# Kernel optimization log

Measured on AMD Instinct MI355X. Metric: run time of the kernel, lower is better.

Reference implementation:

```python
import jax, jax.numpy as jnp
import numpy as np

B, CIN, T, H, W = 1, 256, 64, 32, 32
A, G = 8, 8
SCALES = jnp.array([1., 2., 4., 8., 16., 32., 64., 128.], dtype=jnp.float32)
FEAT_STRIDE = 8.0
NMS_TOP_N = 100
NMS_THRESH = 0.7
MIN_SIZE = 4.0
POS_THR, NEG_THR = 0.7, 0.3
NEG_INF = -1e9


def _conv3d(x, w, b, strides):
    y = jax.lax.conv_general_dilated(
        x, w, window_strides=strides, padding=[(1, 1)] * 3,
        dimension_numbers=('NCDHW', 'OIDHW', 'NCDHW'))
    return y + b[None, :, None, None, None]


def _iou(a, b):
    # 1D interval IoU; a, b broadcastable [..., 2] = (start, end)
    inter = jnp.maximum(jnp.minimum(a[..., 1], b[..., 1]) - jnp.maximum(a[..., 0], b[..., 0]), 0.0)
    union = (a[..., 1] - a[..., 0]) + (b[..., 1] - b[..., 0]) - inter
    return inter / jnp.maximum(union, 1e-6)


def _nms(boxes, scores):
    # greedy 1D NMS: boxes [N,2], scores [N] -> top NMS_TOP_N (zero-padded)
    n = scores.shape[0]
    def step(sc, _):
        i = jnp.argmax(sc)
        s, box = sc[i], boxes[i]
        sup = (_iou(box[None], boxes) > NMS_THRESH) | (jnp.arange(n) == i)
        return jnp.where(sup, NEG_INF, sc), (box, s)
    _, (kb, ks) = jax.lax.scan(step, scores, None, length=NMS_TOP_N)
    keep = ks > NEG_INF * 0.5
    return jnp.where(keep[:, None], kb, 0.0), jnp.where(keep, ks, 0.0)


def _forward(base_feat, gt_chunks, video_len, c1w, c1b, c2w, c2b, sw, sb, dw, db):
    bsz = base_feat.shape[0]
    x = _conv3d(base_feat, c1w, c1b, (1, 2, 2))
    x = _conv3d(x, c2w, c2b, (1, 2, 2))
    feat = jnp.max(x, axis=(3, 4))                       # AdaptiveMaxPool3d((None,1,1)) -> [B,512,T]
    tlen = feat.shape[2]
    score_logit = (jnp.einsum('oc,bct->bot', sw, feat) + sb[None, :, None]).reshape(bsz, 2, A, tlen)
    delta = (jnp.einsum('oc,bct->bot', dw, feat) + db[None, :, None]).reshape(bsz, 2, A, tlen)
    prob = jax.nn.softmax(score_logit, axis=1)
    logp = jax.nn.log_softmax(score_logit, axis=1)

    # anchors: A lengths x T temporal positions, flattened as a*T + t
    anchor_len = FEAT_STRIDE * SCALES                                    # [A]
    centers = (jnp.arange(tlen, dtype=jnp.float32) + 0.5) * FEAT_STRIDE  # [T]
    a_start = centers[None, :] - anchor_len[:, None] / 2                 # [A,T]
    a_end = centers[None, :] + anchor_len[:, None] / 2
    anchors = jnp.stack([a_start, a_end], -1).reshape(-1, 2)             # [N,2]
    N = A * tlen

    # ---- proposal decode + NMS ----
    dc, dl = delta[:, 0], delta[:, 1]                                    # [B,A,T]
    pc = centers[None, None, :] + dc * anchor_len[None, :, None]
    pl = anchor_len[None, :, None] * jnp.exp(jnp.clip(dl, -10.0, 10.0))
    lim = tlen * FEAT_STRIDE
    ps = jnp.clip(pc - pl / 2, 0.0, lim)
    pe = jnp.clip(pc + pl / 2, 0.0, lim)
    boxes = jnp.stack([ps, pe], -1).reshape(bsz, N, 2)
    fg = prob[:, 1].reshape(bsz, N)
    fg = jnp.where((pe - ps).reshape(bsz, N) >= MIN_SIZE, fg, NEG_INF)
    prop_coord, prop_score = jax.vmap(_nms)(boxes, fg)

    # ---- IoU-based label assignment ----
    ious = _iou(anchors[None, :, None, :], gt_chunks[:, None, :, :])     # [B,N,G]
    max_iou = ious.max(-1)
    arg = ious.argmax(-1)                                                # [B,N]
    label = jnp.where(max_iou < NEG_THR, 0, -1)
    label = jnp.where(max_iou >= POS_THR, 1, label)
    best = ious.argmax(1)                                                # best anchor per gt [B,G]
    bidx = jnp.arange(bsz)[:, None]
    label = label.at[bidx, best].set(1)
    vl = video_len.astype(jnp.float32)[:, None]
    inside = (anchors[None, :, 0] >= 0.0) & (anchors[None, :, 1] <= vl)
    label = jnp.where(inside, label, -1)

    matched = gt_chunks[bidx, arg]                                       # [B,N,2]
    gc = (matched[..., 0] + matched[..., 1]) / 2
    gl = jnp.maximum(matched[..., 1] - matched[..., 0], 1e-6)
    ac = (anchors[:, 0] + anchors[:, 1]) / 2
    al = anchors[:, 1] - anchors[:, 0]
    reg_label = jnp.stack([(gc - ac[None]) / al[None], jnp.log(gl / al[None])], -1)
    reg_label = jax.lax.stop_gradient(reg_label)                          # targets carry no grad

    # ---- losses ----
    logp2 = logp.reshape(bsz, 2, N).transpose(0, 2, 1)                   # [B,N,2]
    lab = jnp.maximum(label, 0)
    nll = -jnp.take_along_axis(logp2, lab[..., None], axis=2)[..., 0]
    mask = (label >= 0).astype(jnp.float32)
    cls_loss = (nll * mask).sum() / jnp.maximum(mask.sum(), 1.0)

    delta2 = delta.reshape(bsz, 2, N).transpose(0, 2, 1)                 # [B,N,2]
    d = delta2 - reg_label
    sl1 = jnp.where(jnp.abs(d) < 1.0, 0.5 * d * d, jnp.abs(d) - 0.5).sum(-1)
    pos = (label == 1).astype(jnp.float32)
    reg_loss = (sl1 * pos).sum() / jnp.maximum(pos.sum(), 1.0)
    return prop_coord, prop_score, cls_loss, reg_loss


def setup_inputs() -> dict:
    key = jax.random.key(0)
    ks = jax.random.split(key, 8)
    base_feat = jax.random.normal(ks[0], (B, CIN, T, H, W), jnp.float32)
    starts = jax.random.uniform(ks[1], (B, G), minval=0.0, maxval=448.0)
    lens = jax.random.uniform(ks[2], (B, G), minval=8.0, maxval=64.0)
    gt_chunks = jnp.stack([starts, jnp.clip(starts + lens, 0.0, T * FEAT_STRIDE)], -1)
    video_len = jnp.full((B,), int(T * FEAT_STRIDE), jnp.int32)
    s = 0.02
    return dict(
        base_feat=base_feat, gt_chunks=gt_chunks, video_len=video_len,
        conv1_w=jax.random.normal(ks[3], (512, CIN, 3, 3, 3), jnp.float32) * s,
        conv1_b=jnp.zeros((512,), jnp.float32),
        conv2_w=jax.random.normal(ks[4], (512, 512, 3, 3, 3), jnp.float32) * s,
        conv2_b=jnp.zeros((512,), jnp.float32),
        score_w=jax.random.normal(ks[5], (2 * A, 512), jnp.float32) * s,
        score_b=jnp.zeros((2 * A,), jnp.float32),
        delta_w=jax.random.normal(ks[6], (2 * A, 512), jnp.float32) * s,
        delta_b=jnp.zeros((2 * A,), jnp.float32),
    )


def reference(base_feat, gt_chunks, video_len, conv1_w, conv1_b, conv2_w, conv2_b, score_w, score_b, delta_w, delta_b):
    return _forward(base_feat, gt_chunks, video_len, conv1_w, conv1_b, conv2_w, conv2_b, score_w, score_b, delta_w, delta_b)
```

## Files before the change

kernel.cpp:

```cpp
#include <hip/hip_runtime.h>

typedef __attribute__((ext_vector_type(8))) _Float16 half8;
typedef __attribute__((ext_vector_type(4))) _Float16 half4;
typedef __attribute__((ext_vector_type(4))) float floatx4;

#define DI __device__ __forceinline__

DI void gl_lds16(const void* g, void* l) {
    __builtin_amdgcn_global_load_lds(
        (__attribute__((address_space(1))) void*)(g),
        (__attribute__((address_space(3))) void*)(l), 16, 0, 0);
}


__global__ __launch_bounds__(256) void wt_split_t(
        const float* __restrict__ w1, _Float16* __restrict__ w1I,
        const float* __restrict__ w2, _Float16* __restrict__ w2I,
        float* __restrict__ zp) {
    __shared__ float L[13824];
    const int b = blockIdx.x;
    const int tid = threadIdx.x;
    if (b == 0 && tid < 64) zp[tid] = 0.0f;
    if (b < 512) {
        const float* src = w1 + (size_t)b * 6912;
        for (int idx = tid; idx < 6912; idx += 256) L[idx] = src[idx] * 64.0f;
        __syncthreads();
        for (int c = tid; c < 864; c += 256) {
            const int tap = c >> 5, o = c & 31;
            half8 h, l;
#pragma unroll
            for (int j = 0; j < 8; ++j) {
                const float x = L[(o * 8 + j) * 27 + tap];
                const _Float16 hh = (_Float16)x;
                h[j] = hh; l[j] = (_Float16)(x - (float)hh);
            }
            const size_t off = (size_t)b * 13824 + (size_t)(tap * 8 + (o >> 2)) * 64 + (o & 3) * 8;
            *(half8*)&w1I[off] = h;
            *(half8*)&w1I[off + 32] = l;
        }
    } else {
        const float* src = w2 + (size_t)(b - 512) * 13824;
        for (int idx = tid; idx < 13824; idx += 256) L[idx] = src[idx] * 64.0f;
        __syncthreads();
        for (int c = tid; c < 1728; c += 256) {
            const int tap = c >> 6, o = c & 63;
            half8 h, l;
#pragma unroll
            for (int j = 0; j < 8; ++j) {
                const float x = L[(o * 8 + j) * 27 + tap];
                const _Float16 hh = (_Float16)x;
                h[j] = hh; l[j] = (_Float16)(x - (float)hh);
            }
            const size_t off = (size_t)(b - 512) * 27648 + (size_t)(tap * 16 + (o >> 2)) * 64 + (o & 3) * 8;
            *(half8*)&w2I[off] = h;
            *(half8*)&w2I[off + 32] = l;
        }
    }
}

__global__ __launch_bounds__(256) void in_split(const float* __restrict__ in,
                                                _Float16* __restrict__ oI) {
    __shared__ float T[128 * 65];
    const int hb = blockIdx.x;
    const int s0 = blockIdx.y * 64;
    const int tid = threadIdx.x;
    const int cil = tid >> 1, part = tid & 1;
    const float* src = in + (size_t)(hb * 128 + cil) * 65536 + s0 + part * 32;
    float v[32];
#pragma unroll
    for (int q = 0; q < 8; ++q) *(float4*)(v + q * 4) = *(const float4*)(src + q * 4);
#pragma unroll
    for (int j = 0; j < 32; ++j) T[cil * 65 + part * 32 + j] = v[j];
    __syncthreads();
#pragma unroll
    for (int k = 0; k < 4; ++k) {
        const int c = tid + k * 256;
        const int sp = c >> 4, ol = c & 15;
        half8 h, l;
#pragma unroll
        for (int j = 0; j < 8; ++j) {
            const float x = T[(ol * 8 + j) * 65 + sp];
            const _Float16 hh = (_Float16)x;
            h[j] = hh; l[j] = (_Float16)(x - (float)hh);
        }
        const int og = hb * 16 + ol;
        const size_t off = (size_t)(s0 + sp) * 512 + (size_t)(og >> 2) * 64 + (og & 3) * 8;
        *(half8*)&oI[off] = h;
        *(half8*)&oI[off + 32] = l;
    }
}

__global__ __launch_bounds__(256, 2) void conv1_mfma(
        const _Float16* __restrict__ xI, const _Float16* __restrict__ wI,
        const float* __restrict__ b1, const _Float16* __restrict__ zp,
        _Float16* __restrict__ yI) {
    __shared__ __align__(16) _Float16 A2[2][128 * 64];
    __shared__ __align__(16) _Float16 B2[2][128 * 64];
    const int tid = threadIdx.x;
    const int co_blk = blockIdx.x;
    const int t = blockIdx.y;
    const int h0 = blockIdx.z * 8;
    const int wid = tid >> 6, lane = tid & 63;
    const int wm = wid & 1, wn = wid >> 1;
    const int ml = lane & 15, ql = lane >> 4;
    const int cs0 = (ql ^ (ml & 7)) * 8;
    const int cs1 = ((4 + ql) ^ (ml & 7)) * 8;
    const int sl = lane & 7, rl = lane >> 3;
    const int lc = sl ^ rl;
    size_t aoff[4]; int dstq[4], ih2[4], iw2[4];
    const size_t wbo = (size_t)co_blk * 128 * 13824;
#pragma unroll
    for (int q = 0; q < 4; ++q) {
        const int row = (q * 4 + wid) * 8 + rl;
        aoff[q] = wbo + (size_t)row * 13824 + lc * 8;
        dstq[q] = (q * 4 + wid) * 512 + lane * 8;
        const int h = h0 + (row >> 4), w = row & 15;
        ih2[q] = 2 * h - 1; iw2[q] = 2 * w - 1;
    }

    floatx4 zz = {0.f, 0.f, 0.f, 0.f};
    floatx4 acc[4][4];
#pragma unroll
    for (int i = 0; i < 4; ++i)
#pragma unroll
        for (int j = 0; j < 4; ++j) acc[i][j] = zz;

    auto stage = [&](int kt, int kh, int kw, int cb, int bi) {
        const int tap = (kt * 3 + kh) * 3 + kw;
        const size_t ab = (size_t)(tap * 8 + cb) * 64;
        _Float16* Ad = A2[bi]; _Float16* Bd = B2[bi];
        const int it = t + kt - 1;
        const bool tok = ((unsigned)it < 64u);
#pragma unroll
        for (int q = 0; q < 4; ++q) {
            gl_lds16(wI + aoff[q] + ab, &Ad[dstq[q]]);
            const int ih = ih2[q] + kh, iw = iw2[q] + kw;
            const bool ok = tok && ((unsigned)ih < 32u) && ((unsigned)iw < 32u);
            const _Float16* src = ok
                ? (xI + (size_t)(it * 1024 + ih * 32 + iw) * 512 + cb * 64 + lc * 8)
                : (zp + lc * 8);
            gl_lds16(src, &Bd[dstq[q]]);
        }
    };

    int kt = 0, kh = 0, kw = 0, cb = 0;
    stage(0, 0, 0, 0, 0);
    kw = 1;
    for (int i = 0; i < 216; ++i) {
        __syncthreads();
        if (i + 1 < 216) {
            stage(kt, kh, kw, cb, (i + 1) & 1);
            if (++kw == 3) { kw = 0; if (++kh == 3) { kh = 0; if (++kt == 3) { kt = 0; ++cb; } } }
        }
        const _Float16* Ab = A2[i & 1];
        const _Float16* Bb = B2[i & 1];
        half8 ah[4], alo[4], bh8[4], blo[4];
#pragma unroll
        for (int mi = 0; mi < 4; ++mi) {
            ah[mi]  = *(const half8*)&Ab[(wm * 64 + mi * 16 + ml) * 64 + cs0];
            alo[mi] = *(const half8*)&Ab[(wm * 64 + mi * 16 + ml) * 64 + cs1];
        }
#pragma unroll
        for (int ni = 0; ni < 4; ++ni) {
            bh8[ni] = *(const half8*)&Bb[(wn * 64 + ni * 16 + ml) * 64 + cs0];
            blo[ni] = *(const half8*)&Bb[(wn * 64 + ni * 16 + ml) * 64 + cs1];
        }
#pragma unroll
        for (int mi = 0; mi < 4; ++mi)
#pragma unroll
            for (int ni = 0; ni < 4; ++ni) {
                acc[mi][ni] = __builtin_amdgcn_mfma_f32_16x16x32_f16(ah[mi],  bh8[ni], acc[mi][ni], 0, 0, 0);
                acc[mi][ni] = __builtin_amdgcn_mfma_f32_16x16x32_f16(ah[mi],  blo[ni], acc[mi][ni], 0, 0, 0);
                acc[mi][ni] = __builtin_amdgcn_mfma_f32_16x16x32_f16(alo[mi], bh8[ni], acc[mi][ni], 0, 0, 0);
            }
    }

    const int qr = ql * 4;
#pragma unroll
    for (int mi = 0; mi < 4; ++mi) {
        const int co = co_blk * 128 + wm * 64 + mi * 16 + qr;
#pragma unroll
        for (int ni = 0; ni < 4; ++ni) {
            const int n = wn * 64 + ni * 16 + ml;
            const int h = h0 + (n >> 4), w = n & 15;
            const size_t base = ((size_t)t * 256 + h * 16 + w) * 1024
                              + (size_t)(co >> 5) * 64 + (co & 31);
            half4 hv, lv;
#pragma unroll
            for (int r = 0; r < 4; ++r) {
                const float v = acc[mi][ni][r] * 0.015625f + b1[co + r];
                const _Float16 hb = (_Float16)v;
                hv[r] = hb;
                lv[r] = (_Float16)(v - (float)hb);
            }
            *(half4*)(yI + base) = hv;
            *(half4*)(yI + base + 32) = lv;
        }
    }
}

__global__ __launch_bounds__(256, 2) void conv2_mfma(
        const _Float16* __restrict__ xI, const _Float16* __restrict__ wI,
        const _Float16* __restrict__ zp,
        float* __restrict__ x2p) {
    __shared__ __align__(16) _Float16 A2[2][128 * 64];
    __shared__ __align__(16) _Float16 B2[2][128 * 64];
    const int tid = threadIdx.x;
    const int co_blk = blockIdx.x;
    const int tp = blockIdx.y;
    const int ks = blockIdx.z;
    const int wid = tid >> 6, lane = tid & 63;
    const int wm = wid & 1, wn = wid >> 1;
    const int ml = lane & 15, ql = lane >> 4;
    const int cs0 = (ql ^ (ml & 7)) * 8;
    const int cs1 = ((4 + ql) ^ (ml & 7)) * 8;
    const int sl = lane & 7, rl = lane >> 3;
    const int lc = sl ^ rl;
    size_t aoff[4]; int dstq[4], ih2[4], iw2[4], tl4[4];
    const size_t wbo = (size_t)co_blk * 128 * 27648;
#pragma unroll
    for (int q = 0; q < 4; ++q) {
        const int row = (q * 4 + wid) * 8 + rl;
        aoff[q] = wbo + (size_t)row * 27648 + lc * 8;
        dstq[q] = (q * 4 + wid) * 512 + lane * 8;
        const int sp = row & 63;
        tl4[q] = row >> 6;
        ih2[q] = 2 * (sp >> 3) - 1; iw2[q] = 2 * (sp & 7) - 1;
    }

    floatx4 zz = {0.f, 0.f, 0.f, 0.f};
    floatx4 acc[4][4];
#pragma unroll
    for (int i = 0; i < 4; ++i)
#pragma unroll
        for (int j = 0; j < 4; ++j) acc[i][j] = zz;

    auto stage = [&](int kt, int kh, int kw, int cb, int bi) {
        const int tap = (kt * 3 + kh) * 3 + kw;
        const size_t ab = (size_t)(tap * 16 + cb) * 64;
        _Float16* Ad = A2[bi]; _Float16* Bd = B2[bi];
#pragma unroll
        for (int q = 0; q < 4; ++q) {
            gl_lds16(wI + aoff[q] + ab, &Ad[dstq[q]]);
            const int it = tp * 2 + tl4[q] + kt - 1;
            const int ih = ih2[q] + kh, iw = iw2[q] + kw;
            const bool ok = ((unsigned)it < 64u) && ((unsigned)ih < 16u) && ((unsigned)iw < 16u);
            const _Float16* src = ok
                ? (xI + (size_t)(it * 256 + ih * 16 + iw) * 1024 + cb * 64 + lc * 8)
                : (zp + lc * 8);
            gl_lds16(src, &Bd[dstq[q]]);
        }
    };

    int kt = 0, kh = 0, kw = 0, cb = ks * 4;
    stage(0, 0, 0, cb, 0);
    kw = 1;
    for (int i = 0; i < 108; ++i) {
        __syncthreads();
        if (i + 1 < 108) {
            stage(kt, kh, kw, cb, (i + 1) & 1);
            if (++kw == 3) { kw = 0; if (++kh == 3) { kh = 0; if (++kt == 3) { kt = 0; ++cb; } } }
        }
        const _Float16* Ab = A2[i & 1];
        const _Float16* Bb = B2[i & 1];
        half8 ah[4], alo[4], bh8[4], blo[4];
#pragma unroll
        for (int mi = 0; mi < 4; ++mi) {
            ah[mi]  = *(const half8*)&Ab[(wm * 64 + mi * 16 + ml) * 64 + cs0];
            alo[mi] = *(const half8*)&Ab[(wm * 64 + mi * 16 + ml) * 64 + cs1];
        }
#pragma unroll
        for (int ni = 0; ni < 4; ++ni) {
            bh8[ni] = *(const half8*)&Bb[(wn * 64 + ni * 16 + ml) * 64 + cs0];
            blo[ni] = *(const half8*)&Bb[(wn * 64 + ni * 16 + ml) * 64 + cs1];
        }
#pragma unroll
        for (int mi = 0; mi < 4; ++mi)
#pragma unroll
            for (int ni = 0; ni < 4; ++ni) {
                acc[mi][ni] = __builtin_amdgcn_mfma_f32_16x16x32_f16(ah[mi],  bh8[ni], acc[mi][ni], 0, 0, 0);
                acc[mi][ni] = __builtin_amdgcn_mfma_f32_16x16x32_f16(ah[mi],  blo[ni], acc[mi][ni], 0, 0, 0);
                acc[mi][ni] = __builtin_amdgcn_mfma_f32_16x16x32_f16(alo[mi], bh8[ni], acc[mi][ni], 0, 0, 0);
            }
    }

    const int qr = ql * 4;
#pragma unroll
    for (int mi = 0; mi < 4; ++mi) {
        const int co = co_blk * 128 + wm * 64 + mi * 16 + qr;
#pragma unroll
        for (int ni = 0; ni < 4; ++ni) {
            const int n = wn * 64 + ni * 16 + ml;
            const int ng = tp * 128 + n;
            float4 v;
            v.x = acc[mi][ni][0]; v.y = acc[mi][ni][1];
            v.z = acc[mi][ni][2]; v.w = acc[mi][ni][3];
            *(float4*)&x2p[((size_t)ks * 4096 + ng) * 512 + co] = v;
        }
    }
}

__global__ __launch_bounds__(256) void feat_head(
        const float* __restrict__ x2p, const float* __restrict__ b2,
        const float* __restrict__ sw, const float* __restrict__ sb,
        const float* __restrict__ dw, const float* __restrict__ db,
        float* __restrict__ scoreL, float* __restrict__ deltaL) {
    __shared__ float fr[512];
    __shared__ float partial[32][8];
    const int t = blockIdx.x, tid = threadIdx.x;
#pragma unroll
    for (int cc = 0; cc < 2; ++cc) {
        const int c = tid + cc * 256;
        float mx = -3.4e38f;
        for (int sp = 0; sp < 64; ++sp) {
            const size_t ng = (size_t)t * 64 + sp;
            const float s = x2p[ng * 512 + c]
                          + x2p[((size_t)4096 + ng) * 512 + c]
                          + x2p[((size_t)8192 + ng) * 512 + c]
                          + x2p[((size_t)12288 + ng) * 512 + c];
            mx = fmaxf(mx, s);
        }
        fr[c] = mx * 0.015625f + b2[c];
    }
    __syncthreads();
    const int o = tid & 31, part = tid >> 5;
    const float* wrow = (o < 16) ? (sw + (size_t)o * 512) : (dw + (size_t)(o - 16) * 512);
    float s = 0.f;
    const int j0 = part * 64;
#pragma unroll 16
    for (int j = 0; j < 64; ++j) s += wrow[j0 + j] * fr[j0 + j];
    partial[o][part] = s;
    __syncthreads();
    if (tid < 32) {
        float tot = 0.f;
#pragma unroll
        for (int p = 0; p < 8; ++p) tot += partial[tid][p];
        tot += (tid < 16) ? sb[tid] : db[tid - 16];
        if (tid < 16) scoreL[tid * 64 + t] = tot;
        else deltaL[(tid - 16) * 64 + t] = tot;
    }
}

__global__ void nms_loss_kernel(const float* __restrict__ scoreL,
                                const float* __restrict__ deltaL,
                                const float* __restrict__ gt,
                                const int* __restrict__ video_len,
                                float* __restrict__ out) {
    const int lane = threadIdx.x & 63;
    float gsv[8], gev[8];
#pragma unroll
    for (int g = 0; g < 8; ++g) { gsv[g] = gt[2 * g]; gev[g] = gt[2 * g + 1]; }
    const float center = ((float)lane + 0.5f) * 8.0f;
    float psv[8], pev[8], fg[8], l0v[8], l1v[8], dcv[8], dlv[8];
#pragma unroll
    for (int j = 0; j < 8; ++j) {
        const float s0 = scoreL[j * 64 + lane], s1 = scoreL[(8 + j) * 64 + lane];
        const float mm = fmaxf(s0, s1);
        const float lse = mm + logf(expf(s0 - mm) + expf(s1 - mm));
        l0v[j] = s0 - lse; l1v[j] = s1 - lse;
        const float dc = deltaL[j * 64 + lane], dl = deltaL[(8 + j) * 64 + lane];
        dcv[j] = dc; dlv[j] = dl;
        const float alen = 8.0f * (float)(1 << j);
        const float pc = center + dc * alen;
        const float pl = alen * expf(fminf(fmaxf(dl, -10.0f), 10.0f));
        const float ps = fminf(fmaxf(pc - pl * 0.5f, 0.0f), 512.0f);
        const float pe = fminf(fmaxf(pc + pl * 0.5f, 0.0f), 512.0f);
        psv[j] = ps; pev[j] = pe;
        fg[j] = ((pe - ps) >= 4.0f) ? expf(l1v[j]) : -1e9f;
    }
    for (int itn = 0; itn < 100; ++itn) {
        float v = fg[0]; int idx = lane;
#pragma unroll
        for (int j = 1; j < 8; ++j) if (fg[j] > v) { v = fg[j]; idx = lane + 64 * j; }
#pragma unroll
        for (int off = 32; off > 0; off >>= 1) {
            const float ov = __shfl_down(v, off);
            const int oi = __shfl_down(idx, off);
            if (ov > v || (ov == v && oi < idx)) { v = ov; idx = oi; }
        }
        v = __shfl(v, 0); idx = __shfl(idx, 0);
        const int wj = idx >> 6, wl = idx & 63;
        float bw0 = 0.f, bw1 = 0.f;
#pragma unroll
        for (int j = 0; j < 8; ++j) if (j == wj) { bw0 = psv[j]; bw1 = pev[j]; }
        const float b0 = __shfl(bw0, wl);
        const float b1 = __shfl(bw1, wl);
        if (lane == 0) {
            const bool kept = v > -5e8f;
            out[2 * itn] = kept ? b0 : 0.0f;
            out[2 * itn + 1] = kept ? b1 : 0.0f;
            out[200 + itn] = kept ? v : 0.0f;
        }
#pragma unroll
        for (int j = 0; j < 8; ++j) {
            const int n = lane + 64 * j;
            const float inter = fmaxf(fminf(b1, pev[j]) - fmaxf(b0, psv[j]), 0.0f);
            const float uni = (b1 - b0) + (pev[j] - psv[j]) - inter;
            const float iou = inter / fmaxf(uni, 1e-6f);
            if (iou > 0.7f || n == idx) fg[j] = -1e9f;
        }
    }
    int labv[8], aggv[8];
#pragma unroll
    for (int j = 0; j < 8; ++j) {
        const float alen = 8.0f * (float)(1 << j);
        const float as_ = center - alen * 0.5f, ae_ = center + alen * 0.5f;
        float mx = -1.0f; int ag = 0;
#pragma unroll
        for (int g = 0; g < 8; ++g) {
            const float inter = fmaxf(fminf(ae_, gev[g]) - fmaxf(as_, gsv[g]), 0.0f);
            const float uni = (ae_ - as_) + (gev[g] - gsv[g]) - inter;
            const float iou = inter / fmaxf(uni, 1e-6f);
            if (iou > mx) { mx = iou; ag = g; }
        }
        labv[j] = (mx < 0.3f) ? 0 : ((mx >= 0.7f) ? 1 : -1);
        aggv[j] = ag;
    }
    for (int g = 0; g < 8; ++g) {
        float v = -1.0f; int idx = 0;
#pragma unroll
        for (int j = 0; j < 8; ++j) {
            const int n = lane + 64 * j;
            const float alen = 8.0f * (float)(1 << j);
            const float as_ = center - alen * 0.5f, ae_ = center + alen * 0.5f;
            const float inter = fmaxf(fminf(ae_, gev[g]) - fmaxf(as_, gsv[g]), 0.0f);
            const float uni = (ae_ - as_) + (gev[g] - gsv[g]) - inter;
            const float iou = inter / fmaxf(uni, 1e-6f);
            if (iou > v || (iou == v && n < idx)) { v = iou; idx = n; }
        }
#pragma unroll
        for (int off = 32; off > 0; off >>= 1) {
            const float ov = __shfl_down(v, off);
            const int oi = __shfl_down(idx, off);
            if (ov > v || (ov == v && oi < idx)) { v = ov; idx = oi; }
        }
        idx = __shfl(idx, 0);
#pragma unroll
        for (int j = 0; j < 8; ++j)
            if (lane == (idx & 63) && j == (idx >> 6)) labv[j] = 1;
    }
    const float vl = (float)video_len[0];
    float nll_s = 0.f, msk_s = 0.f, reg_s = 0.f, pos_s = 0.f;
#pragma unroll
    for (int j = 0; j < 8; ++j) {
        const float alen = 8.0f * (float)(1 << j);
        const float as_ = center - alen * 0.5f, ae_ = center + alen * 0.5f;
        int l = labv[j];
        if (!((as_ >= 0.0f) && (ae_ <= vl))) l = -1;
        if (l >= 0) {
            msk_s += 1.0f;
            nll_s -= (l == 1) ? l1v[j] : l0v[j];
            if (l == 1) {
                pos_s += 1.0f;
                float gcv = 0.f, glv = 0.f;
#pragma unroll
                for (int g = 0; g < 8; ++g)
                    if (g == aggv[j]) {
                        gcv = (gsv[g] + gev[g]) * 0.5f;
                        glv = fmaxf(gev[g] - gsv[g], 1e-6f);
                    }
                const float r0 = (gcv - center) / alen;
                const float r1 = logf(glv / alen);
                const float d0 = dcv[j] - r0, d1 = dlv[j] - r1;
                float s = (fabsf(d0) < 1.0f) ? (0.5f * d0 * d0) : (fabsf(d0) - 0.5f);
                s += (fabsf(d1) < 1.0f) ? (0.5f * d1 * d1) : (fabsf(d1) - 0.5f);
                reg_s += s;
            }
        }
    }
    float sums[4] = {nll_s, msk_s, reg_s, pos_s};
#pragma unroll
    for (int k = 0; k < 4; ++k)
#pragma unroll
        for (int off = 32; off > 0; off >>= 1) sums[k] += __shfl_down(sums[k], off);
    if (lane == 0) {
        out[300] = sums[0] / fmaxf(sums[1], 1.0f);
        out[301] = sums[2] / fmaxf(sums[3], 1.0f);
    }
}

extern "C" void kernel_launch(void* const* d_in, const int* in_sizes, int n_in,
                              void* d_out, int out_size, void* d_ws, size_t ws_size,
                              hipStream_t stream) {
    const float* base_feat = (const float*)d_in[0];
    const float* gt        = (const float*)d_in[1];
    const int*   video_len = (const int*)d_in[2];
    const float* w1        = (const float*)d_in[3];
    const float* b1        = (const float*)d_in[4];
    const float* w2        = (const float*)d_in[5];
    const float* b2        = (const float*)d_in[6];
    const float* sw        = (const float*)d_in[7];
    const float* sb        = (const float*)d_in[8];
    const float* dw        = (const float*)d_in[9];
    const float* db        = (const float*)d_in[10];

    char* ws = (char*)d_ws;
    _Float16* w1I = (_Float16*)ws;  ws += (size_t)512 * 13824 * 2;
    _Float16* w2I = (_Float16*)ws;  ws += (size_t)512 * 27648 * 2;
    _Float16* inI = (_Float16*)ws;  ws += (size_t)65536 * 512 * 2;
    _Float16* x1I = (_Float16*)ws;  ws += (size_t)16384 * 1024 * 2;
    float* scoreL = (float*)ws;     ws += (size_t)16 * 64 * 4;
    float* deltaL = (float*)ws;     ws += (size_t)16 * 64 * 4;
    float* zpage  = (float*)ws;     ws += (size_t)64 * 4;
    float* x2p = (float*)inI;

    wt_split_t<<<1024, 256, 0, stream>>>(w1, w1I, w2, w2I, zpage);
    in_split<<<dim3(2, 1024), 256, 0, stream>>>(base_feat, inI);
    conv1_mfma<<<dim3(4, 64, 2), 256, 0, stream>>>(inI, w1I, b1,
                                                   (const _Float16*)zpage, x1I);
    conv2_mfma<<<dim3(4, 32, 4), 256, 0, stream>>>(x1I, w2I,
                                                   (const _Float16*)zpage, x2p);
    feat_head<<<64, 256, 0, stream>>>(x2p, b2, sw, sb, dw, db, scoreL, deltaL);
    nms_loss_kernel<<<1, 64, 0, stream>>>(scoreL, deltaL, gt, video_len,
                                          (float*)d_out);
}
```

Before: 772.0 us.

## Switch conv kernels to 32x32x16 MFMA tiles with hoisted address math

```diff
diff --git a/kernel.cpp b/kernel.cpp
--- a/kernel.cpp
+++ b/kernel.cpp
@@ -2,7 +2,7 @@
 
 typedef __attribute__((ext_vector_type(8))) _Float16 half8;
 typedef __attribute__((ext_vector_type(4))) _Float16 half4;
-typedef __attribute__((ext_vector_type(4))) float floatx4;
+typedef __attribute__((ext_vector_type(16))) float floatx16;
 
 #define DI __device__ __forceinline__
 
@@ -102,100 +102,126 @@
     const int h0 = blockIdx.z * 8;
     const int wid = tid >> 6, lane = tid & 63;
     const int wm = wid & 1, wn = wid >> 1;
-    const int ml = lane & 15, ql = lane >> 4;
-    const int cs0 = (ql ^ (ml & 7)) * 8;
-    const int cs1 = ((4 + ql) ^ (ml & 7)) * 8;
+    const int r5 = lane & 31, h5 = lane >> 5, l7 = lane & 7;
     const int sl = lane & 7, rl = lane >> 3;
     const int lc = sl ^ rl;
-    size_t aoff[4]; int dstq[4], ih2[4], iw2[4];
+
+    const _Float16* wA[4]; const _Float16* bB[4];
+    int dstq[4]; bool hok[4], wok[4];
     const size_t wbo = (size_t)co_blk * 128 * 13824;
 #pragma unroll
     for (int q = 0; q < 4; ++q) {
         const int row = (q * 4 + wid) * 8 + rl;
-        aoff[q] = wbo + (size_t)row * 13824 + lc * 8;
+        wA[q] = wI + wbo + (size_t)row * 13824 + lc * 8;
         dstq[q] = (q * 4 + wid) * 512 + lane * 8;
         const int h = h0 + (row >> 4), w = row & 15;
-        ih2[q] = 2 * h - 1; iw2[q] = 2 * w - 1;
-    }
-
-    floatx4 zz = {0.f, 0.f, 0.f, 0.f};
-    floatx4 acc[4][4];
-#pragma unroll
-    for (int i = 0; i < 4; ++i)
-#pragma unroll
-        for (int j = 0; j < 4; ++j) acc[i][j] = zz;
-
-    auto stage = [&](int kt, int kh, int kw, int cb, int bi) {
-        const int tap = (kt * 3 + kh) * 3 + kw;
-        const size_t ab = (size_t)(tap * 8 + cb) * 64;
-        _Float16* Ad = A2[bi]; _Float16* Bd = B2[bi];
+        const int ih2 = 2 * h - 1, iw2 = 2 * w - 1;
+        hok[q] = (ih2 >= 0); wok[q] = (iw2 >= 0);
+        bB[q] = xI + (ptrdiff_t)(ih2 * 32 + iw2) * 512 + lc * 8;
+    }
+    const _Float16* zpl = zp + lc * 8;
+    const int cs0 = (h5 ^ l7) * 8;
+
+    floatx16 acc[2][2];
+#pragma unroll
+    for (int mi = 0; mi < 2; ++mi)
+#pragma unroll
+        for (int ni = 0; ni < 2; ++ni)
+#pragma unroll
+            for (int e = 0; e < 16; ++e) acc[mi][ni][e] = 0.0f;
+
+    auto stage = [&](int kt, int cb, int KH, int KW, _Float16* Ad, _Float16* Bd) {
         const int it = t + kt - 1;
         const bool tok = ((unsigned)it < 64u);
+        const size_t ab = (size_t)(((kt * 9 + KH * 3 + KW) * 8 + cb) * 64);
+        const ptrdiff_t boff = (ptrdiff_t)it * 524288 + KH * 16384 + KW * 512 + cb * 64;
 #pragma unroll
         for (int q = 0; q < 4; ++q) {
-            gl_lds16(wI + aoff[q] + ab, &Ad[dstq[q]]);
-            const int ih = ih2[q] + kh, iw = iw2[q] + kw;
-            const bool ok = tok && ((unsigned)ih < 32u) && ((unsigned)iw < 32u);
-            const _Float16* src = ok
-                ? (xI + (size_t)(it * 1024 + ih * 32 + iw) * 512 + cb * 64 + lc * 8)
-                : (zp + lc * 8);
-            gl_lds16(src, &Bd[dstq[q]]);
+            gl_lds16(wA[q] + ab, &Ad[dstq[q]]);
+            const bool ok = tok && (KH > 0 || hok[q]) && (KW > 0 || wok[q]);
+            const _Float16* s = ok ? (bB[q] + boff) : zpl;
+            gl_lds16(s, &Bd[dstq[q]]);
         }
     };
 
-    int kt = 0, kh = 0, kw = 0, cb = 0;
-    stage(0, 0, 0, 0, 0);
-    kw = 1;
-    for (int i = 0; i < 216; ++i) {
-        __syncthreads();
-        if (i + 1 < 216) {
-            stage(kt, kh, kw, cb, (i + 1) & 1);
-            if (++kw == 3) { kw = 0; if (++kh == 3) { kh = 0; if (++kt == 3) { kt = 0; ++cb; } } }
-        }
-        const _Float16* Ab = A2[i & 1];
-        const _Float16* Bb = B2[i & 1];
-        half8 ah[4], alo[4], bh8[4], blo[4];
-#pragma unroll
-        for (int mi = 0; mi < 4; ++mi) {
-            ah[mi]  = *(const half8*)&Ab[(wm * 64 + mi * 16 + ml) * 64 + cs0];
-            alo[mi] = *(const half8*)&Ab[(wm * 64 + mi * 16 + ml) * 64 + cs1];
-        }
-#pragma unroll
-        for (int ni = 0; ni < 4; ++ni) {
-            bh8[ni] = *(const half8*)&Bb[(wn * 64 + ni * 16 + ml) * 64 + cs0];
-            blo[ni] = *(const half8*)&Bb[(wn * 64 + ni * 16 + ml) * 64 + cs1];
-        }
-#pragma unroll
-        for (int mi = 0; mi < 4; ++mi)
-#pragma unroll
-            for (int ni = 0; ni < 4; ++ni) {
-                acc[mi][ni] = __builtin_amdgcn_mfma_f32_16x16x32_f16(ah[mi],  bh8[ni], acc[mi][ni], 0, 0, 0);
-                acc[mi][ni] = __builtin_amdgcn_mfma_f32_16x16x32_f16(ah[mi],  blo[ni], acc[mi][ni], 0, 0, 0);
-                acc[mi][ni] = __builtin_amdgcn_mfma_f32_16x16x32_f16(alo[mi], bh8[ni], acc[mi][ni], 0, 0, 0);
-            }
-    }
-
-    const int qr = ql * 4;
-#pragma unroll
-    for (int mi = 0; mi < 4; ++mi) {
-        const int co = co_blk * 128 + wm * 64 + mi * 16 + qr;
-#pragma unroll
-        for (int ni = 0; ni < 4; ++ni) {
-            const int n = wn * 64 + ni * 16 + ml;
-            const int h = h0 + (n >> 4), w = n & 15;
-            const size_t base = ((size_t)t * 256 + h * 16 + w) * 1024
-                              + (size_t)(co >> 5) * 64 + (co & 31);
-            half4 hv, lv;
-#pragma unroll
-            for (int r = 0; r < 4; ++r) {
-                const float v = acc[mi][ni][r] * 0.015625f + b1[co + r];
-                const _Float16 hb = (_Float16)v;
-                hv[r] = hb;
-                lv[r] = (_Float16)(v - (float)hb);
-            }
-            *(half4*)(yI + base) = hv;
-            *(half4*)(yI + base + 32) = lv;
-        }
+    stage(0, 0, 0, 0, A2[0], B2[0]);
+    for (int o = 0; o < 24; ++o) {
+        const int cb = o / 3, kt = o - cb * 3;
+#pragma unroll
+        for (int j = 0; j < 9; ++j) {
+            __syncthreads();
+            const int par = (o + j) & 1;
+            if (j < 8) {
+                stage(kt, cb, (j + 1) / 3, (j + 1) % 3, A2[par ^ 1], B2[par ^ 1]);
+            } else if (o < 23) {
+                stage((o + 1) % 3, (o + 1) / 3, 0, 0, A2[par ^ 1], B2[par ^ 1]);
+            }
+            const _Float16* Ab = A2[par];
+            const _Float16* Bb = B2[par];
+            half8 a_h[2][2], a_l[2][2], b_h[2][2], b_l[2][2];
+#pragma unroll
+            for (int mi = 0; mi < 2; ++mi) {
+                const _Float16* pa = &Ab[(wm * 64 + mi * 32 + r5) * 64];
+                const _Float16* pb = &Bb[(wn * 64 + mi * 32 + r5) * 64];
+#pragma unroll
+                for (int k = 0; k < 2; ++k) {
+                    const int cs = cs0 ^ (k * 16);
+                    a_h[mi][k] = *(const half8*)&pa[cs];
+                    a_l[mi][k] = *(const half8*)&pa[cs ^ 32];
+                    b_h[mi][k] = *(const half8*)&pb[cs];
+                    b_l[mi][k] = *(const half8*)&pb[cs ^ 32];
+                }
+            }
+            __builtin_amdgcn_s_setprio(1);
+#pragma unroll
+            for (int k = 0; k < 2; ++k) {
+#pragma unroll
+                for (int mi = 0; mi < 2; ++mi)
+#pragma unroll
+                    for (int ni = 0; ni < 2; ++ni)
+                        acc[mi][ni] = __builtin_amdgcn_mfma_f32_32x32x16_f16(
+                            a_h[mi][k], b_h[ni][k], acc[mi][ni], 0, 0, 0);
+#pragma unroll
+                for (int mi = 0; mi < 2; ++mi)
+#pragma unroll
+                    for (int ni = 0; ni < 2; ++ni)
+                        acc[mi][ni] = __builtin_amdgcn_mfma_f32_32x32x16_f16(
+                            a_h[mi][k], b_l[ni][k], acc[mi][ni], 0, 0, 0);
+#pragma unroll
+                for (int mi = 0; mi < 2; ++mi)
+#pragma unroll
+                    for (int ni = 0; ni < 2; ++ni)
+                        acc[mi][ni] = __builtin_amdgcn_mfma_f32_32x32x16_f16(
+                            a_l[mi][k], b_h[ni][k], acc[mi][ni], 0, 0, 0);
+            }
+            __builtin_amdgcn_s_setprio(0);
+        }
+    }
+
+#pragma unroll
+    for (int ni = 0; ni < 2; ++ni) {
+        const int n = wn * 64 + ni * 32 + r5;
+        const int h = h0 + (n >> 4), w = n & 15;
+        const size_t spb = ((size_t)t * 256 + h * 16 + w) * 1024;
+#pragma unroll
+        for (int mi = 0; mi < 2; ++mi)
+#pragma unroll
+            for (int g = 0; g < 4; ++g) {
+                const int co = co_blk * 128 + wm * 64 + mi * 32 + g * 8 + h5 * 4;
+                const float4 bv = *(const float4*)&b1[co];
+                half4 hv, lv;
+#pragma unroll
+                for (int r = 0; r < 4; ++r) {
+                    const float bb = (r == 0) ? bv.x : (r == 1) ? bv.y : (r == 2) ? bv.z : bv.w;
+                    const float v = acc[mi][ni][g * 4 + r] * 0.015625f + bb;
+                    const _Float16 hb = (_Float16)v;
+                    hv[r] = hb;
+                    lv[r] = (_Float16)(v - (float)hb);
+                }
+                const size_t base = spb + (size_t)(co >> 5) * 64 + (co & 31);
+                *(half4*)(yI + base) = hv;
+                *(half4*)(yI + base + 32) = lv;
+            }
     }
 }
 
@@ -211,92 +237,116 @@
     const int ks = blockIdx.z;
     const int wid = tid >> 6, lane = tid & 63;
     const int wm = wid & 1, wn = wid >> 1;
-    const int ml = lane & 15, ql = lane >> 4;
-    const int cs0 = (ql ^ (ml & 7)) * 8;
-    const int cs1 = ((4 + ql) ^ (ml & 7)) * 8;
+    const int r5 = lane & 31, h5 = lane >> 5, l7 = lane & 7;
     const int sl = lane & 7, rl = lane >> 3;
     const int lc = sl ^ rl;
-    size_t aoff[4]; int dstq[4], ih2[4], iw2[4], tl4[4];
+
+    const _Float16* wA[4]; const _Float16* bB[4];
+    int dstq[4], itv[4]; bool hok[4], wok[4];
     const size_t wbo = (size_t)co_blk * 128 * 27648;
 #pragma unroll
     for (int q = 0; q < 4; ++q) {
         const int row = (q * 4 + wid) * 8 + rl;
-        aoff[q] = wbo + (size_t)row * 27648 + lc * 8;
+        wA[q] = wI + wbo + (size_t)row * 27648 + lc * 8;
         dstq[q] = (q * 4 + wid) * 512 + lane * 8;
         const int sp = row & 63;
-        tl4[q] = row >> 6;
-        ih2[q] = 2 * (sp >> 3) - 1; iw2[q] = 2 * (sp & 7) - 1;
-    }
-
-    floatx4 zz = {0.f, 0.f, 0.f, 0.f};
-    floatx4 acc[4][4];
-#pragma unroll
-    for (int i = 0; i < 4; ++i)
-#pragma unroll
-        for (int j = 0; j < 4; ++j) acc[i][j] = zz;
-
-    auto stage = [&](int kt, int kh, int kw, int cb, int bi) {
-        const int tap = (kt * 3 + kh) * 3 + kw;
-        const size_t ab = (size_t)(tap * 16 + cb) * 64;
-        _Float16* Ad = A2[bi]; _Float16* Bd = B2[bi];
+        itv[q] = tp * 2 + (row >> 6) - 1;
+        const int ih2 = 2 * (sp >> 3) - 1, iw2 = 2 * (sp & 7) - 1;
+        hok[q] = (ih2 >= 0); wok[q] = (iw2 >= 0);
+        bB[q] = xI + (ptrdiff_t)((itv[q] * 256 + ih2 * 16 + iw2) * 1024) + lc * 8;
+    }
+    const _Float16* zpl = zp + lc * 8;
+    const int cs0 = (h5 ^ l7) * 8;
+
+    floatx16 acc[2][2];
+#pragma unroll
+    for (int mi = 0; mi < 2; ++mi)
+#pragma unroll
+        for (int ni = 0; ni < 2; ++ni)
+#pragma unroll
+            for (int e = 0; e < 16; ++e) acc[mi][ni][e] = 0.0f;
+
+    auto stage = [&](int kt, int cb, int KH, int KW, _Float16* Ad, _Float16* Bd) {
+        const size_t ab = (size_t)(((kt * 9 + KH * 3 + KW) * 16 + cb) * 64);
+        const ptrdiff_t boff = (ptrdiff_t)kt * 262144 + KH * 16384 + KW * 1024 + cb * 64;
 #pragma unroll
         for (int q = 0; q < 4; ++q) {
-            gl_lds16(wI + aoff[q] + ab, &Ad[dstq[q]]);
-            const int it = tp * 2 + tl4[q] + kt - 1;
-            const int ih = ih2[q] + kh, iw = iw2[q] + kw;
-            const bool ok = ((unsigned)it < 64u) && ((unsigned)ih < 16u) && ((unsigned)iw < 16u);
-            const _Float16* src = ok
-                ? (xI + (size_t)(it * 256 + ih * 16 + iw) * 1024 + cb * 64 + lc * 8)
-                : (zp + lc * 8);
-            gl_lds16(src, &Bd[dstq[q]]);
+            gl_lds16(wA[q] + ab, &Ad[dstq[q]]);
+            const bool ok = ((unsigned)(itv[q] + kt) < 64u)
+                         && (KH > 0 || hok[q]) && (KW > 0 || wok[q]);
+            const _Float16* s = ok ? (bB[q] + boff) : zpl;
+            gl_lds16(s, &Bd[dstq[q]]);
         }
     };
 
-    int kt = 0, kh = 0, kw = 0, cb = ks * 4;
-    stage(0, 0, 0, cb, 0);
-    kw = 1;
-    for (int i = 0; i < 108; ++i) {
-        __syncthreads();
-        if (i + 1 < 108) {
-            stage(kt, kh, kw, cb, (i + 1) & 1);
-            if (++kw == 3) { kw = 0; if (++kh == 3) { kh = 0; if (++kt == 3) { kt = 0; ++cb; } } }
-        }
-        const _Float16* Ab = A2[i & 1];
-        const _Float16* Bb = B2[i & 1];
-        half8 ah[4], alo[4], bh8[4], blo[4];
-#pragma unroll
-        for (int mi = 0; mi < 4; ++mi) {
-            ah[mi]  = *(const half8*)&Ab[(wm * 64 + mi * 16 + ml) * 64 + cs0];
-            alo[mi] = *(const half8*)&Ab[(wm * 64 + mi * 16 + ml) * 64 + cs1];
-        }
-#pragma unroll
-        for (int ni = 0; ni < 4; ++ni) {
-            bh8[ni] = *(const half8*)&Bb[(wn * 64 + ni * 16 + ml) * 64 + cs0];
-            blo[ni] = *(const half8*)&Bb[(wn * 64 + ni * 16 + ml) * 64 + cs1];
-        }
-#pragma unroll
-        for (int mi = 0; mi < 4; ++mi)
-#pragma unroll
-            for (int ni = 0; ni < 4; ++ni) {
-                acc[mi][ni] = __builtin_amdgcn_mfma_f32_16x16x32_f16(ah[mi],  bh8[ni], acc[mi][ni], 0, 0, 0);
-                acc[mi][ni] = __builtin_amdgcn_mfma_f32_16x16x32_f16(ah[mi],  blo[ni], acc[mi][ni], 0, 0, 0);
-                acc[mi][ni] = __builtin_amdgcn_mfma_f32_16x16x32_f16(alo[mi], bh8[ni], acc[mi][ni], 0, 0, 0);
-            }
-    }
-
-    const int qr = ql * 4;
-#pragma unroll
-    for (int mi = 0; mi < 4; ++mi) {
-        const int co = co_blk * 128 + wm * 64 + mi * 16 + qr;
-#pragma unroll
-        for (int ni = 0; ni < 4; ++ni) {
-            const int n = wn * 64 + ni * 16 + ml;
-            const int ng = tp * 128 + n;
-            float4 v;
-            v.x = acc[mi][ni][0]; v.y = acc[mi][ni][1];
-            v.z = acc[mi][ni][2]; v.w = acc[mi][ni][3];
-            *(float4*)&x2p[((size_t)ks * 4096 + ng) * 512 + co] = v;
-        }
+    stage(0, ks * 4, 0, 0, A2[0], B2[0]);
+    for (int o = 0; o < 12; ++o) {
+        const int kt = o % 3, cb = ks * 4 + o / 3;
+#pragma unroll
+        for (int j = 0; j < 9; ++j) {
+            __syncthreads();
+            const int par = (o + j) & 1;
+            if (j < 8) {
+                stage(kt, cb, (j + 1) / 3, (j + 1) % 3, A2[par ^ 1], B2[par ^ 1]);
+            } else if (o < 11) {
+                stage((o + 1) % 3, ks * 4 + (o + 1) / 3, 0, 0, A2[par ^ 1], B2[par ^ 1]);
+            }
+            const _Float16* Ab = A2[par];
+            const _Float16* Bb = B2[par];
+            half8 a_h[2][2], a_l[2][2], b_h[2][2], b_l[2][2];
+#pragma unroll
+            for (int mi = 0; mi < 2; ++mi) {
+                const _Float16* pa = &Ab[(wm * 64 + mi * 32 + r5) * 64];
+                const _Float16* pb = &Bb[(wn * 64 + mi * 32 + r5) * 64];
+#pragma unroll
+                for (int k = 0; k < 2; ++k) {
+                    const int cs = cs0 ^ (k * 16);
+                    a_h[mi][k] = *(const half8*)&pa[cs];
+                    a_l[mi][k] = *(const half8*)&pa[cs ^ 32];
+                    b_h[mi][k] = *(const half8*)&pb[cs];
+                    b_l[mi][k] = *(const half8*)&pb[cs ^ 32];
+                }
+            }
+            __builtin_amdgcn_s_setprio(1);
+#pragma unroll
+            for (int k = 0; k < 2; ++k) {
+#pragma unroll
+                for (int mi = 0; mi < 2; ++mi)
+#pragma unroll
+                    for (int ni = 0; ni < 2; ++ni)
+                        acc[mi][ni] = __builtin_amdgcn_mfma_f32_32x32x16_f16(
+                            a_h[mi][k], b_h[ni][k], acc[mi][ni], 0, 0, 0);
+#pragma unroll
+                for (int mi = 0; mi < 2; ++mi)
+#pragma unroll
+                    for (int ni = 0; ni < 2; ++ni)
+                        acc[mi][ni] = __builtin_amdgcn_mfma_f32_32x32x16_f16(
+                            a_h[mi][k], b_l[ni][k], acc[mi][ni], 0, 0, 0);
+#pragma unroll
+                for (int mi = 0; mi < 2; ++mi)
+#pragma unroll
+                    for (int ni = 0; ni < 2; ++ni)
+                        acc[mi][ni] = __builtin_amdgcn_mfma_f32_32x32x16_f16(
+                            a_l[mi][k], b_h[ni][k], acc[mi][ni], 0, 0, 0);
+            }
+            __builtin_amdgcn_s_setprio(0);
+        }
+    }
+
+#pragma unroll
+    for (int ni = 0; ni < 2; ++ni) {
+        const int n = wn * 64 + ni * 32 + r5;
+        const size_t rb = ((size_t)ks * 4096 + tp * 128 + n) * 512;
+#pragma unroll
+        for (int mi = 0; mi < 2; ++mi)
+#pragma unroll
+            for (int g = 0; g < 4; ++g) {
+                const int co = co_blk * 128 + wm * 64 + mi * 32 + g * 8 + h5 * 4;
+                float4 v;
+                v.x = acc[mi][ni][g * 4 + 0]; v.y = acc[mi][ni][g * 4 + 1];
+                v.z = acc[mi][ni][g * 4 + 2]; v.w = acc[mi][ni][g * 4 + 3];
+                *(float4*)&x2p[rb + co] = v;
+            }
     }
 }
 
```

Result: slower. 841.3 us (+9.0%).
